# Kernel tuning notes

Measured on AMD Instinct MI355X. Metric: run time of the kernel, lower is better.

## Reference

```python
import jax, jax.numpy as jnp
import numpy as np

EMB_DIM = 512
N_HEAD = 8
HEAD_DIM = EMB_DIM // N_HEAD
SEQ_LEN = 2048
BATCH = 4


def setup_inputs() -> dict:
    key = jax.random.key(0)
    k1, k2, k3 = jax.random.split(key, 3)
    emb = jax.random.normal(k1, (SEQ_LEN, BATCH, EMB_DIM), dtype=jnp.float32)
    # torch Linear weight layout: (out_features, in_features)
    W = jax.random.normal(k2, (3 * EMB_DIM, EMB_DIM), dtype=jnp.float32) * 0.02
    b = jax.random.normal(k3, (3 * EMB_DIM,), dtype=jnp.float32) * 0.02
    return {"emb": emb, "W": W, "b": b}


def reference(emb, W, b):
    L, B, E = emb.shape
    scaling = (E / N_HEAD) ** -0.5
    # qkv projection: (L, B, 3E)
    ft = jnp.einsum('lbe,oe->lbo', emb, W) + b
    # interleaved per-head qkv split, matching reshape(L, B*nh, -1).chunk(3, -1)
    ft = ft.reshape(L, B * N_HEAD, 3 * HEAD_DIM).transpose(1, 0, 2)  # (B*nh, L, 3*hd)
    q, k, v = jnp.split(ft, 3, axis=-1)  # each (B*nh, L, hd)
    # attention scores with value-based zero mask
    scores = jnp.einsum('bld,bmd->blm', q, k) * scaling  # (B*nh, L, L)
    mask = scores == 0
    scores = jnp.where(mask, -jnp.inf, scores)
    attn = jax.nn.softmax(scores, axis=-1)
    attn = jnp.where(mask, jnp.zeros((), attn.dtype), attn)
    out = jnp.einsum('blm,bmd->bld', attn, v)  # (B*nh, L, hd)
    out = out.transpose(1, 0, 2).reshape(L, B, E)
    return out
```

## Files before the change

### kernel.cpp

```cpp
#include <hip/hip_runtime.h>
#include <hip/hip_bf16.h>
#include <cstdint>
#include <math.h>


typedef __bf16 bf16x8 __attribute__((ext_vector_type(8)));
typedef float  f32x4  __attribute__((ext_vector_type(4)));
typedef float  f32x16 __attribute__((ext_vector_type(16)));
typedef unsigned int uint32x4 __attribute__((ext_vector_type(4)));

#define MFMA16(a, b, c) __builtin_amdgcn_mfma_f32_16x16x32_bf16(a, b, c, 0, 0, 0)
#define MFMA32(a, b, c) __builtin_amdgcn_mfma_f32_32x32x16_bf16(a, b, c, 0, 0, 0)

#define EXP2F(x) __builtin_amdgcn_exp2f(x)

#define QSCALE 0.18033688011112042f

enum {
  LSEQ = 2048,
  NBATCH = 4,
  EMB = 512,
  NHEAD = 8,
  HDIM = 64,
  NBH = NBATCH * NHEAD,
  MROWS = LSEQ * NBATCH,
  KDIM = EMB,
  NOUT = 3 * EMB
};

__device__ inline void gload_lds16(const void* g, void* l) {
  __builtin_amdgcn_global_load_lds(
      (__attribute__((address_space(1))) void*)(uintptr_t)g,
      (__attribute__((address_space(3))) void*)(uint32_t)(uintptr_t)l,
      16, 0, 0);
}

__device__ inline unsigned packbf(float a, float b) {
  unsigned short ua = __builtin_bit_cast(unsigned short, (__bf16)a);
  unsigned short ub = __builtin_bit_cast(unsigned short, (__bf16)b);
  return (unsigned)ua | ((unsigned)ub << 16);
}

__device__ inline bf16x8 frag_from(unsigned w0, unsigned w1, unsigned w2, unsigned w3) {
  uint32x4 v = {w0, w1, w2, w3};
  return __builtin_bit_cast(bf16x8, v);
}

__global__ __launch_bounds__(256) void cvt2_kernel(const float* __restrict__ a,
                                                   __bf16* __restrict__ oa, int na8,
                                                   const float* __restrict__ b,
                                                   __bf16* __restrict__ ob, int nb8) {
  int i = blockIdx.x * 256 + threadIdx.x;
  const float* in;
  __bf16* out;
  int idx;
  if (i < na8) {
    in = a; out = oa; idx = i;
  } else {
    idx = i - na8;
    if (idx >= nb8) return;
    in = b; out = ob;
  }
  const float4* p = (const float4*)in + (size_t)idx * 2;
  float4 x = p[0], y = p[1];
  bf16x8 o;
  o[0] = (__bf16)x.x; o[1] = (__bf16)x.y; o[2] = (__bf16)x.z; o[3] = (__bf16)x.w;
  o[4] = (__bf16)y.x; o[5] = (__bf16)y.y; o[6] = (__bf16)y.z; o[7] = (__bf16)y.w;
  *(bf16x8*)(out + (size_t)idx * 8) = o;
}

__global__ __launch_bounds__(256) void qkv_gemm_kernel(
    const __bf16* __restrict__ A, const __bf16* __restrict__ Bt,
    const float* __restrict__ bias,
    __bf16* __restrict__ Qh, __bf16* __restrict__ Kh, __bf16* __restrict__ Vth) {
  __shared__ __align__(16) __bf16 As[128 * 64];
  __shared__ __align__(16) __bf16 Bs[128 * 64];

  const int tid = threadIdx.x;
  const int wid = tid >> 6, lane = tid & 63;
  const int g = lane >> 4, lx = lane & 15;
  const int mtile = blockIdx.y, ntile = blockIdx.x;
  const int wm = (wid >> 1) * 64, wn = (wid & 1) * 64;

  const int lr = lane >> 3;
  const int lc = (lane & 7) * 8;

  f32x4 acc[4][4] = {};

  const int rowA0 = mtile * 128;
  const int rowB0 = ntile * 128;

  for (int k0 = 0; k0 < KDIM; k0 += 64) {
#pragma unroll
    for (int i = 0; i < 4; ++i) {
      int chunk = wid * 4 + i;
      gload_lds16(A + (size_t)(rowA0 + chunk * 8 + lr) * KDIM + k0 + lc,
                  As + chunk * 512);
      gload_lds16(Bt + (size_t)(rowB0 + chunk * 8 + lr) * KDIM + k0 + lc,
                  Bs + chunk * 512);
    }
    __syncthreads();
#pragma unroll
    for (int kk = 0; kk < 2; ++kk) {
      bf16x8 af[4], bfr[4];
#pragma unroll
      for (int t = 0; t < 4; ++t)
        af[t] = *(const bf16x8*)&As[(wm + t * 16 + lx) * 64 + kk * 32 + g * 8];
#pragma unroll
      for (int t = 0; t < 4; ++t)
        bfr[t] = *(const bf16x8*)&Bs[(wn + t * 16 + lx) * 64 + kk * 32 + g * 8];
#pragma unroll
      for (int mi = 0; mi < 4; ++mi)
#pragma unroll
        for (int ni = 0; ni < 4; ++ni)
          acc[mi][ni] = MFMA16(af[mi], bfr[ni], acc[mi][ni]);
    }
    __syncthreads();
  }

#pragma unroll
  for (int ni = 0; ni < 4; ++ni) {
    int o = ntile * 128 + wn + ni * 16 + lx;
    float bv = bias[o];
    unsigned h = (unsigned)o / 192u;
    unsigned w = (unsigned)o - h * 192u;
#pragma unroll
    for (int mi = 0; mi < 4; ++mi) {
#pragma unroll
      for (int r = 0; r < 4; ++r) {
        int m = mtile * 128 + wm + mi * 16 + g * 4 + r;
        int l = m >> 2, b = m & 3;
        float v = acc[mi][ni][r] + bv;
        int bh = b * NHEAD + (int)h;
        if (w < 64u) {
          Qh[((size_t)bh * LSEQ + l) * HDIM + w] = (__bf16)(v * QSCALE);
        } else if (w < 128u) {
          Kh[((size_t)bh * LSEQ + l) * HDIM + (w - 64u)] = (__bf16)v;
        } else {
          Vth[((size_t)bh * HDIM + (w - 128u)) * LSEQ + l] = (__bf16)v;
        }
      }
    }
  }
}

__global__ __launch_bounds__(512, 2) void attn_kernel(const __bf16* __restrict__ Qh,
                                                      const __bf16* __restrict__ Kh,
                                                      const __bf16* __restrict__ Vth,
                                                      float* __restrict__ out) {
  __shared__ __align__(16) __bf16 Ks[4][64 * 64];
  __shared__ __align__(16) __bf16 Vs[4][64 * 64];

  const int flat = blockIdx.x;
  const int sw = (flat & 7) * 64 + (flat >> 3);
  const int bh = sw >> 4, qt = sw & 15;
  const int tid = threadIdx.x, wid = tid >> 6, lane = tid & 63;
  const int pair = wid >> 1, role = wid & 1;
  const int ql = lane & 31, hi = lane >> 5;
  const int rb = ql & 7;

  const __bf16* Kb = Kh + (size_t)bh * (LSEQ * HDIM);
  const __bf16* Vb = Vth + (size_t)bh * (HDIM * LSEQ);

  const __bf16* Qp =
      Qh + ((size_t)bh * LSEQ + qt * 128 + pair * 32 + ql) * HDIM + hi * 8;
  bf16x8 qf[4];
#pragma unroll
  for (int s = 0; s < 4; ++s) qf[s] = *(const bf16x8*)(Qp + s * 16);

  const int lr3 = lane >> 3;
  const int ch = (lane & 7) ^ lr3;

#define STAGE_T(tt)                                                        \
  {                                                                        \
    const int tn_ = (tt) & 31;                                             \
    const int b_ = tn_ & 3;                                                \
    gload_lds16(Kb + (size_t)(tn_ * 64 + wid * 8 + lr3) * HDIM + ch * 8,   \
                &Ks[b_][(wid * 8) * 64]);                                  \
    gload_lds16(Vb + (size_t)(wid * 8 + lr3) * LSEQ + tn_ * 64 + ch * 8,   \
                &Vs[b_][(wid * 8) * 64]);                                  \
  }

  int ko[4], vo[4];
#pragma unroll
  for (int fs = 0; fs < 4; ++fs)
    ko[fs] = (role * 32 + ql) * 64 + (((2 * fs + hi) ^ rb) << 3);
#pragma unroll
  for (int dt = 0; dt < 2; ++dt)
#pragma unroll
    for (int ks = 0; ks < 2; ++ks)
      vo[dt * 2 + ks] =
          (dt * 32 + ql) * 64 + (((role * 4 + 2 * ks + hi) ^ rb) << 3);

  f32x16 ot[2] = {};
  float lacc[8] = {};
  bf16x8 pfA[2], pfB[2];

#define HEAD                                           \
  asm volatile("s_waitcnt vmcnt(2)" ::: "memory");     \
  __builtin_amdgcn_s_barrier();                        \
  asm volatile("" ::: "memory");

#define FILL(pfX, s_)                                                        \
  {                                                                          \
    const int cur_ = (s_) & 3;                                               \
    const __bf16* kr_ = &Ks[cur_][0];                                        \
    bf16x8 k0 = *(const bf16x8*)(kr_ + ko[0]);                               \
    bf16x8 k1 = *(const bf16x8*)(kr_ + ko[1]);                               \
    bf16x8 k2 = *(const bf16x8*)(kr_ + ko[2]);                               \
    bf16x8 k3 = *(const bf16x8*)(kr_ + ko[3]);                               \
    f32x16 st_ = {};                                                         \
    __builtin_amdgcn_s_setprio(1);                                           \
    st_ = MFMA32(k0, qf[0], st_);                                            \
    st_ = MFMA32(k1, qf[1], st_);                                            \
    st_ = MFMA32(k2, qf[2], st_);                                            \
    st_ = MFMA32(k3, qf[3], st_);                                            \
    __builtin_amdgcn_s_setprio(0);                                           \
    _Pragma("unroll") for (int r = 0; r < 16; ++r) {                         \
      float e_ = EXP2F(st_[r]);                                              \
      st_[r] = e_;                                                           \
      lacc[r & 7] += e_;                                                     \
    }                                                                        \
    unsigned b0 = packbf(st_[0], st_[1]), b1 = packbf(st_[2], st_[3]);       \
    unsigned b2 = packbf(st_[4], st_[5]), b3 = packbf(st_[6], st_[7]);       \
    unsigned b4 = packbf(st_[8], st_[9]), b5 = packbf(st_[10], st_[11]);     \
    unsigned b6 = packbf(st_[12], st_[13]), b7 = packbf(st_[14], st_[15]);   \
    asm("v_permlane32_swap_b32 %0, %1" : "+v"(b0), "+v"(b2));                \
    asm("v_permlane32_swap_b32 %0, %1" : "+v"(b1), "+v"(b3));                \
    asm("v_permlane32_swap_b32 %0, %1" : "+v"(b4), "+v"(b6));                \
    asm("v_permlane32_swap_b32 %0, %1" : "+v"(b5), "+v"(b7));                \
    pfX[0] = frag_from(b0, b1, b2, b3);                                      \
    pfX[1] = frag_from(b4, b5, b6, b7);                                      \
  }

#define PVSTEP(pfX, bidx)                                  \
  {                                                        \
    const __bf16* vr_ = &Vs[bidx][0];                      \
    bf16x8 v0 = *(const bf16x8*)(vr_ + vo[0]);             \
    bf16x8 v1 = *(const bf16x8*)(vr_ + vo[1]);             \
    bf16x8 v2 = *(const bf16x8*)(vr_ + vo[2]);             \
    bf16x8 v3 = *(const bf16x8*)(vr_ + vo[3]);             \
    __builtin_amdgcn_s_setprio(1);                         \
    ot[0] = MFMA32(v0, pfX[0], ot[0]);                     \
    ot[0] = MFMA32(v1, pfX[1], ot[0]);                     \
    ot[1] = MFMA32(v2, pfX[0], ot[1]);                     \
    ot[1] = MFMA32(v3, pfX[1], ot[1]);                     \
    __builtin_amdgcn_s_setprio(0);                         \
  }

  STAGE_T(0);
  STAGE_T(1);

  HEAD;
  FILL(pfA, 0);
  STAGE_T(2);

  HEAD;
  FILL(pfB, 1);
  PVSTEP(pfA, 0);
  STAGE_T(3);

  for (int i = 0; i < 15; ++i) {
    const int s0 = 2 + 2 * i;
    HEAD;
    FILL(pfA, s0);
    PVSTEP(pfB, (s0 - 1) & 3);
    STAGE_T(s0 + 2);
    HEAD;
    FILL(pfB, s0 + 1);
    PVSTEP(pfA, s0 & 3);
    STAGE_T(s0 + 3);
  }
  PVSTEP(pfB, 3);

#undef STAGE_T
#undef HEAD
#undef FILL
#undef PVSTEP

  float ls = 0.f;
#pragma unroll
  for (int r = 0; r < 8; ++r) ls += lacc[r];
  ls += __shfl_xor(ls, 32);

  asm volatile("s_waitcnt vmcnt(0) lgkmcnt(0)" ::: "memory");
  __syncthreads();
  float* stash_ot = (float*)&Ks[0][0];
  float* stash_ls = (float*)&Vs[0][0];
  float* myo = stash_ot + (wid * 64 + lane) * 16;
  f32x16 give = role ? ot[0] : ot[1];
#pragma unroll
  for (int g4 = 0; g4 < 4; ++g4) {
    float4 v4 = make_float4(give[4 * g4 + 0], give[4 * g4 + 1],
                            give[4 * g4 + 2], give[4 * g4 + 3]);
    *(float4*)(myo + 4 * g4) = v4;
  }
  stash_ls[wid * 64 + lane] = ls;
  __syncthreads();

  const float* po = stash_ot + ((wid ^ 1) * 64 + lane) * 16;
  f32x16 mine = role ? ot[1] : ot[0];
#pragma unroll
  for (int r = 0; r < 16; ++r) mine[r] += po[r];
  const float lst = ls + stash_ls[(wid ^ 1) * 64 + lane];
  const float inv = 1.f / lst;

  const int lq = qt * 128 + pair * 32 + ql;
  float* ob = out + (size_t)lq * (NBATCH * EMB) + (bh >> 3) * EMB + (bh & 7) * HDIM;
#pragma unroll
  for (int g4 = 0; g4 < 4; ++g4) {
    float4 v4 = make_float4(mine[4 * g4 + 0] * inv, mine[4 * g4 + 1] * inv,
                            mine[4 * g4 + 2] * inv, mine[4 * g4 + 3] * inv);
    *(float4*)(ob + role * 32 + g4 * 8 + hi * 4) = v4;
  }
}

extern "C" void kernel_launch(void* const* d_in, const int* in_sizes, int n_in,
                              void* d_out, int out_size, void* d_ws, size_t ws_size,
                              hipStream_t stream) {
  const float* emb = (const float*)d_in[0];
  const float* W = (const float*)d_in[1];
  const float* bias = (const float*)d_in[2];
  float* out = (float*)d_out;

  char* ws = (char*)d_ws;
  __bf16* embh = (__bf16*)(ws);
  __bf16* Wh   = (__bf16*)(ws + 8388608);
  __bf16* Qh   = (__bf16*)(ws + 9961472);
  __bf16* Kh   = (__bf16*)(ws + 18350080);
  __bf16* Vth  = (__bf16*)(ws + 26738688);

  const int na8 = MROWS * KDIM / 8;
  const int nb8 = NOUT * KDIM / 8;
  cvt2_kernel<<<dim3((na8 + nb8 + 255) / 256), dim3(256), 0, stream>>>(
      emb, embh, na8, W, Wh, nb8);
  qkv_gemm_kernel<<<dim3(NOUT / 128, MROWS / 128), dim3(256), 0, stream>>>(
      embh, Wh, bias, Qh, Kh, Vth);
  attn_kernel<<<dim3(NBH * (LSEQ / 128)), dim3(512), 0, stream>>>(Qh, Kh, Vth, out);
}
```

Baseline: 93.16 us.

## Remap QKV GEMM rows per batch with XCD-aware tiling and vectorized V stores

```diff
diff --git a/kernel.cpp b/kernel.cpp
--- a/kernel.cpp
+++ b/kernel.cpp
@@ -79,22 +79,28 @@
   const int tid = threadIdx.x;
   const int wid = tid >> 6, lane = tid & 63;
   const int g = lane >> 4, lx = lane & 15;
-  const int mtile = blockIdx.y, ntile = blockIdx.x;
+
+  const int orig = blockIdx.x;
+  const int xcd = orig & 7, rr = orig >> 3;
+  const int mt_local = rr / 12;
+  const int ntile = rr - mt_local * 12;
+  const int mtile = xcd * 8 + mt_local;
+  const int b = mtile >> 4;
+  const int l0 = (mtile & 15) * 128;
+
   const int wm = (wid >> 1) * 64, wn = (wid & 1) * 64;
-
   const int lr = lane >> 3;
   const int lc = (lane & 7) * 8;
 
   f32x4 acc[4][4] = {};
 
-  const int rowA0 = mtile * 128;
   const int rowB0 = ntile * 128;
 
   for (int k0 = 0; k0 < KDIM; k0 += 64) {
 #pragma unroll
     for (int i = 0; i < 4; ++i) {
       int chunk = wid * 4 + i;
-      gload_lds16(A + (size_t)(rowA0 + chunk * 8 + lr) * KDIM + k0 + lc,
+      gload_lds16(A + ((size_t)(l0 + chunk * 8 + lr) * NBATCH + b) * KDIM + k0 + lc,
                   As + chunk * 512);
       gload_lds16(Bt + (size_t)(rowB0 + chunk * 8 + lr) * KDIM + k0 + lc,
                   Bs + chunk * 512);
@@ -124,21 +130,24 @@
     float bv = bias[o];
     unsigned h = (unsigned)o / 192u;
     unsigned w = (unsigned)o - h * 192u;
+    const size_t bh = (size_t)(b * NHEAD) + h;
 #pragma unroll
     for (int mi = 0; mi < 4; ++mi) {
-#pragma unroll
-      for (int r = 0; r < 4; ++r) {
-        int m = mtile * 128 + wm + mi * 16 + g * 4 + r;
-        int l = m >> 2, b = m & 3;
-        float v = acc[mi][ni][r] + bv;
-        int bh = b * NHEAD + (int)h;
-        if (w < 64u) {
-          Qh[((size_t)bh * LSEQ + l) * HDIM + w] = (__bf16)(v * QSCALE);
-        } else if (w < 128u) {
-          Kh[((size_t)bh * LSEQ + l) * HDIM + (w - 64u)] = (__bf16)v;
-        } else {
-          Vth[((size_t)bh * HDIM + (w - 128u)) * LSEQ + l] = (__bf16)v;
-        }
+      const int l = l0 + wm + mi * 16 + g * 4;
+      if (w < 64u) {
+#pragma unroll
+        for (int r = 0; r < 4; ++r)
+          Qh[(bh * LSEQ + l + r) * HDIM + w] =
+              (__bf16)((acc[mi][ni][r] + bv) * QSCALE);
+      } else if (w < 128u) {
+#pragma unroll
+        for (int r = 0; r < 4; ++r)
+          Kh[(bh * LSEQ + l + r) * HDIM + (w - 64u)] = (__bf16)(acc[mi][ni][r] + bv);
+      } else {
+        unsigned u0 = packbf(acc[mi][ni][0] + bv, acc[mi][ni][1] + bv);
+        unsigned u1 = packbf(acc[mi][ni][2] + bv, acc[mi][ni][3] + bv);
+        uint2 uv = make_uint2(u0, u1);
+        *(uint2*)&Vth[(bh * HDIM + (w - 128u)) * LSEQ + l] = uv;
       }
     }
   }
@@ -334,7 +343,7 @@
   const int nb8 = NOUT * KDIM / 8;
   cvt2_kernel<<<dim3((na8 + nb8 + 255) / 256), dim3(256), 0, stream>>>(
       emb, embh, na8, W, Wh, nb8);
-  qkv_gemm_kernel<<<dim3(NOUT / 128, MROWS / 128), dim3(256), 0, stream>>>(
+  qkv_gemm_kernel<<<dim3(768), dim3(256), 0, stream>>>(
       embh, Wh, bias, Qh, Kh, Vth);
   attn_kernel<<<dim3(NBH * (LSEQ / 128)), dim3(512), 0, stream>>>(Qh, Kh, Vth, out);
 }
```

Result: faster. 88.91 us (-4.6%).
